# Optimization experiments

Measured on AMD Instinct MI355X. Metric: run time of the kernel, lower is better.

Reference implementation:

```python
import jax, jax.numpy as jnp
import numpy as np

OUT, IN, GS = 16384, 4096, 16
G = OUT * IN // GS  # 4194304 groups


def setup_inputs() -> dict:
    key = jax.random.key(0)
    k1, k2, k3, k4 = jax.random.split(key, 4)
    x = jax.random.normal(k1, (8, 32, IN), dtype=jnp.float32)
    weight_q2 = jax.random.randint(k2, (G, GS // 4), 0, 256, dtype=jnp.int32)
    weight_norm = jax.random.uniform(k3, (G, 1), dtype=jnp.float16)
    bias = jax.random.normal(k4, (OUT,), dtype=jnp.float32)
    return {"x": x, "weight_q2": weight_q2, "weight_norm": weight_norm, "bias": bias}


def _dequant_2bit(weight_q2, weight_norm):
    # torch: xq_out[:, i::4] = (xq >> 2i) & 3  =>  element index within group = i + 4*k
    # where k = packed column (slow, stride 4), i = shift index (fast).
    norm = weight_norm.astype(jnp.float32)                      # [G, 1]
    shifts = jnp.arange(4, dtype=jnp.int32) * 2                 # [4]
    vals = (weight_q2[:, :, None] >> shifts) & 3                # [G, 4(pack k), 4(shift i)]
    xq_out = vals.astype(jnp.float32).reshape(G, GS)            # [G, 16], layout k*4 + i
    w = (xq_out / 3.0) * (2.0 * norm) - norm                    # [G, 16]
    return w.reshape(OUT, IN)


def reference(x, weight_q2, weight_norm, bias):
    w = _dequant_2bit(weight_q2, weight_norm)                   # [OUT, IN] fp32
    return jnp.einsum('bsi,oi->bso', x, w) + bias
```

## Files before the change

kernel.cpp:

```cpp
#include <hip/hip_runtime.h>
#include <stdint.h>

#define M_DIM 256
#define N_DIM 16384
#define K_DIM 4096
#define BM 128
#define BN 64
#define BK 64

typedef __bf16 bf16x8 __attribute__((ext_vector_type(8)));
typedef float  f32x4  __attribute__((ext_vector_type(4)));

__device__ __forceinline__ uint32_t f2bf(float f) {
  uint32_t u = __float_as_uint(f);
  return (u + 0x7fffu + ((u >> 16) & 1u)) >> 16;
}

__global__ __launch_bounds__(256) void cvt_x_kernel(const float* __restrict__ x,
                                                    uint4* __restrict__ ws) {
  int T = blockIdx.x * 256 + threadIdx.x;
  int mb_glob = T >> 13;
  int r       = T & 8191;
  int kch     = r >> 6;
  int L       = r & 63;
  int row = mb_glob * 16 + (L & 15);
  int k   = kch * 32 + (L >> 4) * 8;
  const float* p = x + (size_t)row * K_DIM + k;
  float4 a = *(const float4*)p;
  float4 b = *(const float4*)(p + 4);
  uint4 o;
  o.x = f2bf(a.x) | (f2bf(a.y) << 16);
  o.y = f2bf(a.z) | (f2bf(a.w) << 16);
  o.z = f2bf(b.x) | (f2bf(b.y) << 16);
  o.w = f2bf(b.z) | (f2bf(b.w) << 16);
  ws[T] = o;
}

__global__ __launch_bounds__(256, 2) void gemm2bit_kernel(
    const uint4*    __restrict__ aws,
    const uint32_t* __restrict__ q2,
    const float*    __restrict__ nrm,
    const float*    __restrict__ bias,
    float*          __restrict__ out)
{
  __shared__ uint4 Ab[1024];
  __shared__ uint4 Bb[512];

  const int tid  = threadIdx.x;
  const int lane = tid & 63;
  const int w    = tid >> 6;
  const int wm   = w >> 1;
  const int wn   = w & 1;
  const int lo4  = lane & 15;
  const int qd   = lane >> 4;

  const int n0 = blockIdx.x * BN;
  const int m0 = blockIdx.y * BM;

  const int snb  = tid >> 6;
  const int sqd  = (tid >> 4) & 3;
  const int slo4 = tid & 15;
  const int grow = n0 + snb * 16 + slo4;

  f32x4 acc[4][2];
#pragma unroll
  for (int s = 0; s < 4; ++s)
#pragma unroll
    for (int u = 0; u < 2; ++u)
      acc[s][u] = (f32x4){0.f, 0.f, 0.f, 0.f};

  for (int kc = 0; kc < K_DIM; kc += BK) {
    __syncthreads();

#pragma unroll
    for (int j = 0; j < 4; ++j) {
      int s_lin = j * 256 + tid;
      int ca = s_lin >> 6;
      int L  = s_lin & 63;
      int ts = ca >> 3, mb = ca & 7;
      uint4 g = aws[((size_t)(blockIdx.y * 8 + mb) * 128 + (kc >> 5) + ts) * 64 + L];
      Ab[ca * 64 + L] = g;
    }

    {
      int gidx = grow * 256 + (kc >> 4) + sqd;
      uint4 q  = *(const uint4*)(q2 + (size_t)gidx * 4);
      float nv = nrm[gidx];
      float a  = nv * (2.0f / 3.0f);
      float b  = -nv;
      uint32_t res[8];
#pragma unroll
      for (int p = 0; p < 4; ++p) {
        uint32_t qq = (&q.x)[p];
        float f0 = fmaf((float)(qq & 3u), a, b);
        float f1 = fmaf((float)((qq >> 2) & 3u), a, b);
        float f2 = fmaf((float)((qq >> 4) & 3u), a, b);
        float f3 = fmaf((float)((qq >> 6) & 3u), a, b);
        res[p * 2]     = f2bf(f0) | (f2bf(f1) << 16);
        res[p * 2 + 1] = f2bf(f2) | (f2bf(f3) << 16);
      }
      int cb   = (sqd >> 1) * 4 + snb;
      int base = cb * 64 + (sqd & 1) * 32 + slo4;
      Bb[base]      = make_uint4(res[0], res[1], res[2], res[3]);
      Bb[base + 16] = make_uint4(res[4], res[5], res[6], res[7]);
    }

    __syncthreads();

#pragma unroll
    for (int ts = 0; ts < 2; ++ts) {
      bf16x8 af[4], bf[2];
#pragma unroll
      for (int s = 0; s < 4; ++s)
        af[s] = *(const bf16x8*)&Ab[(ts * 8 + wm * 4 + s) * 64 + lane];
#pragma unroll
      for (int u = 0; u < 2; ++u)
        bf[u] = *(const bf16x8*)&Bb[(ts * 4 + wn * 2 + u) * 64 + lane];
#pragma unroll
      for (int s = 0; s < 4; ++s)
#pragma unroll
        for (int u = 0; u < 2; ++u)
          acc[s][u] = __builtin_amdgcn_mfma_f32_16x16x32_bf16(
              af[s], bf[u], acc[s][u], 0, 0, 0);
    }
  }

  float bv[2];
#pragma unroll
  for (int u = 0; u < 2; ++u)
    bv[u] = bias[n0 + wn * 32 + u * 16 + lo4];

#pragma unroll
  for (int s = 0; s < 4; ++s) {
    int mrow = m0 + wm * 64 + s * 16 + qd * 4;
#pragma unroll
    for (int u = 0; u < 2; ++u) {
      int ncol = n0 + wn * 32 + u * 16 + lo4;
      float* p = out + (size_t)mrow * N_DIM + ncol;
#pragma unroll
      for (int r = 0; r < 4; ++r)
        p[(size_t)r * N_DIM] = acc[s][u][r] + bv[u];
    }
  }
}

extern "C" void kernel_launch(void* const* d_in, const int* in_sizes, int n_in,
                              void* d_out, int out_size, void* d_ws, size_t ws_size,
                              hipStream_t stream) {
  const float*    x    = (const float*)d_in[0];
  const uint32_t* q2   = (const uint32_t*)d_in[1];
  const float*    nm   = (const float*)d_in[2];
  const float*    bias = (const float*)d_in[3];
  float*          out  = (float*)d_out;
  uint4*          aws  = (uint4*)d_ws;

  cvt_x_kernel<<<512, 256, 0, stream>>>(x, aws);

  dim3 grid(N_DIM / BN, M_DIM / BM);
  gemm2bit_kernel<<<grid, 256, 0, stream>>>(aws, q2, nm, bias, out);
}
```

Measured before the change: 178.5 us.

## Double BK, register-prefetch next tile, and dequantize via byte-permute lookup

Doubles the K tile to 128 and prefetches the next iteration's activation and quantized weight loads into registers while the MFMAs run on the current tile, so global-load latency overlaps compute. The 2-bit dequantization changes from per-element int-to-float conversion, FMA and rounding to a precomputed bf16 lookup table of the four level values, indexed with v_perm byte selects. This adds register pressure from the prefetch buffers and doubles shared memory, which can lower occupancy. The lookup encodes the four levels as ±norm and ±norm/3 rounded to bf16 directly, which may differ slightly in rounding from the previous FMA path.

```diff
diff --git a/kernel.cpp b/kernel.cpp
--- a/kernel.cpp
+++ b/kernel.cpp
@@ -6,7 +6,8 @@
 #define K_DIM 4096
 #define BM 128
 #define BN 64
-#define BK 64
+#define BK 128
+#define NIT (K_DIM / BK)
 
 typedef __bf16 bf16x8 __attribute__((ext_vector_type(8)));
 typedef float  f32x4  __attribute__((ext_vector_type(4)));
@@ -43,24 +44,23 @@
     const float*    __restrict__ bias,
     float*          __restrict__ out)
 {
-  __shared__ uint4 Ab[1024];
-  __shared__ uint4 Bb[512];
+  __shared__ uint4 Ab[2048];
+  __shared__ uint4 Bb[1024];
 
   const int tid  = threadIdx.x;
-  const int lane = tid & 63;
+  const int l    = tid & 63;
   const int w    = tid >> 6;
   const int wm   = w >> 1;
   const int wn   = w & 1;
-  const int lo4  = lane & 15;
-  const int qd   = lane >> 4;
+  const int lo4  = l & 15;
+  const int qd   = l >> 4;
 
   const int n0 = blockIdx.x * BN;
   const int m0 = blockIdx.y * BM;
 
-  const int snb  = tid >> 6;
-  const int sqd  = (tid >> 4) & 3;
-  const int slo4 = tid & 15;
-  const int grow = n0 + snb * 16 + slo4;
+  const int srow = lo4 + w * 16;
+  const int sgk0 = qd;
+  const int grow = n0 + srow;
 
   f32x4 acc[4][2];
 #pragma unroll
@@ -69,53 +69,77 @@
     for (int u = 0; u < 2; ++u)
       acc[s][u] = (f32x4){0.f, 0.f, 0.f, 0.f};
 
-  for (int kc = 0; kc < K_DIM; kc += BK) {
-    __syncthreads();
+  uint4 pA[8];
+  uint4 pQ[2];
+  float pN[2];
 
+  const int mrow_base = blockIdx.y * 8;
+
+#define LOAD_A(IT)                                                          \
+  _Pragma("unroll") for (int j = 0; j < 8; ++j) {                           \
+    int s_lin = j * 256 + tid;                                              \
+    int c = s_lin >> 6, L = s_lin & 63;                                     \
+    pA[j] = aws[((size_t)(mrow_base + (c & 7)) * 128 + (IT)*4 + (c >> 3)) * 64 + L]; \
+  }
+#define LOAD_B(IT)                                                          \
+  _Pragma("unroll") for (int g = 0; g < 2; ++g) {                           \
+    int gidx = grow * 256 + (IT)*8 + sgk0 + 4 * g;                          \
+    pQ[g] = *(const uint4*)(q2 + (size_t)gidx * 4);                         \
+    pN[g] = nrm[gidx];                                                      \
+  }
+
+  LOAD_A(0)
+  LOAD_B(0)
+
+  for (int it = 0; it < NIT; ++it) {
+    uint32_t rw[16];
 #pragma unroll
-    for (int j = 0; j < 4; ++j) {
-      int s_lin = j * 256 + tid;
-      int ca = s_lin >> 6;
-      int L  = s_lin & 63;
-      int ts = ca >> 3, mb = ca & 7;
-      uint4 g = aws[((size_t)(blockIdx.y * 8 + mb) * 128 + (kc >> 5) + ts) * 64 + L];
-      Ab[ca * 64 + L] = g;
-    }
-
-    {
-      int gidx = grow * 256 + (kc >> 4) + sqd;
-      uint4 q  = *(const uint4*)(q2 + (size_t)gidx * 4);
-      float nv = nrm[gidx];
-      float a  = nv * (2.0f / 3.0f);
-      float b  = -nv;
-      uint32_t res[8];
+    for (int g = 0; g < 2; ++g) {
+      float nv = pN[g];
+      uint32_t u3 = f2bf(nv);
+      uint32_t u1 = f2bf(nv * 0.33333334f);
+      uint32_t T01 = (u3 | (u1 << 16)) ^ 0x80008000u;
+      uint32_t T23 = u1 | (u3 << 16);
 #pragma unroll
       for (int p = 0; p < 4; ++p) {
-        uint32_t qq = (&q.x)[p];
-        float f0 = fmaf((float)(qq & 3u), a, b);
-        float f1 = fmaf((float)((qq >> 2) & 3u), a, b);
-        float f2 = fmaf((float)((qq >> 4) & 3u), a, b);
-        float f3 = fmaf((float)((qq >> 6) & 3u), a, b);
-        res[p * 2]     = f2bf(f0) | (f2bf(f1) << 16);
-        res[p * 2 + 1] = f2bf(f2) | (f2bf(f3) << 16);
+        uint32_t qq = (&pQ[g].x)[p];
+        uint32_t v01 = (qq & 3u) | ((qq & 0x0Cu) << 14);
+        uint32_t v23 = ((qq >> 4) & 3u) | ((qq & 0xC0u) << 10);
+        rw[g * 8 + p * 2]     = __builtin_amdgcn_perm(T23, T01, v01 * 0x0202u + 0x01000100u);
+        rw[g * 8 + p * 2 + 1] = __builtin_amdgcn_perm(T23, T01, v23 * 0x0202u + 0x01000100u);
       }
-      int cb   = (sqd >> 1) * 4 + snb;
-      int base = cb * 64 + (sqd & 1) * 32 + slo4;
-      Bb[base]      = make_uint4(res[0], res[1], res[2], res[3]);
-      Bb[base + 16] = make_uint4(res[4], res[5], res[6], res[7]);
     }
 
     __syncthreads();
 
 #pragma unroll
-    for (int ts = 0; ts < 2; ++ts) {
+    for (int j = 0; j < 8; ++j)
+      Ab[j * 256 + tid] = pA[j];
+
+#pragma unroll
+    for (int g = 0; g < 2; ++g) {
+      int sgk  = sgk0 + 4 * g;
+      int base = ((sgk >> 1) * 4 + w) * 64 + (sgk & 1) * 32 + lo4;
+      Bb[base]      = make_uint4(rw[g * 8 + 0], rw[g * 8 + 1], rw[g * 8 + 2], rw[g * 8 + 3]);
+      Bb[base + 16] = make_uint4(rw[g * 8 + 4], rw[g * 8 + 5], rw[g * 8 + 6], rw[g * 8 + 7]);
+    }
+
+    __syncthreads();
+
+    if (it + 1 < NIT) {
+      LOAD_A(it + 1)
+      LOAD_B(it + 1)
+    }
+
+#pragma unroll
+    for (int ts = 0; ts < 4; ++ts) {
       bf16x8 af[4], bf[2];
 #pragma unroll
       for (int s = 0; s < 4; ++s)
-        af[s] = *(const bf16x8*)&Ab[(ts * 8 + wm * 4 + s) * 64 + lane];
+        af[s] = *(const bf16x8*)&Ab[(ts * 8 + wm * 4 + s) * 64 + l];
 #pragma unroll
       for (int u = 0; u < 2; ++u)
-        bf[u] = *(const bf16x8*)&Bb[(ts * 4 + wn * 2 + u) * 64 + lane];
+        bf[u] = *(const bf16x8*)&Bb[(ts * 4 + wn * 2 + u) * 64 + l];
 #pragma unroll
       for (int s = 0; s < 4; ++s)
 #pragma unroll
@@ -124,6 +148,8 @@
               af[s], bf[u], acc[s][u], 0, 0, 0);
     }
   }
+#undef LOAD_A
+#undef LOAD_B
 
   float bv[2];
 #pragma unroll
```

New measurement: 299.2 us. 1.68x slower.

## Prefetch next K-tile into registers and dequantize 2-bit weights via byte-permute lookup

Applied to the files above, without the earlier changes.

The loads for the next K tile of activations and packed weights are now issued into registers before the current tile's MFMA work, so global-memory latency overlaps with compute. The dequantization that did four FMAs plus bf16 rounding per weight is replaced by a table of four bf16 values (±norm, ±norm/3) built once per tile and selected with v_perm byte shuffles. This adds register pressure under launch bounds of 2 blocks per CU. The lookup's rounding of norm/3 may differ slightly from the original FMA path.

```diff
diff --git a/kernel.cpp b/kernel.cpp
--- a/kernel.cpp
+++ b/kernel.cpp
@@ -47,12 +47,12 @@
   __shared__ uint4 Bb[512];
 
   const int tid  = threadIdx.x;
-  const int lane = tid & 63;
+  const int l    = tid & 63;
   const int w    = tid >> 6;
   const int wm   = w >> 1;
   const int wn   = w & 1;
-  const int lo4  = lane & 15;
-  const int qd   = lane >> 4;
+  const int lo4  = l & 15;
+  const int qd   = l >> 4;
 
   const int n0 = blockIdx.x * BN;
   const int m0 = blockIdx.y * BM;
@@ -69,53 +69,72 @@
     for (int u = 0; u < 2; ++u)
       acc[s][u] = (f32x4){0.f, 0.f, 0.f, 0.f};
 
+  uint4 pA[4];
+  uint4 pQ;
+  float pN;
+
+#define LOAD_B(KC)                                              \
+  {                                                             \
+    int gidx = grow * 256 + ((KC) >> 4) + sqd;                  \
+    pQ = *(const uint4*)(q2 + (size_t)gidx * 4);                \
+    pN = nrm[gidx];                                             \
+  }
+#define LOAD_A(KC)                                                            \
+  _Pragma("unroll") for (int j = 0; j < 4; ++j) {                             \
+    int s_lin = j * 256 + tid;                                                \
+    int ca = s_lin >> 6, L = s_lin & 63;                                      \
+    pA[j] = aws[((size_t)(blockIdx.y * 8 + (ca & 7)) * 128 + ((KC) >> 5) +    \
+                 (ca >> 3)) * 64 + L];                                        \
+  }
+
+  LOAD_B(0)
+  LOAD_A(0)
+
   for (int kc = 0; kc < K_DIM; kc += BK) {
+    uint32_t rw[8];
+    {
+      uint32_t u3 = f2bf(pN);
+      uint32_t u1 = f2bf(pN * 0.33333334f);
+      uint32_t T01 = (u3 | (u1 << 16)) ^ 0x80008000u;
+      uint32_t T23 = u1 | (u3 << 16);
+#pragma unroll
+      for (int p = 0; p < 4; ++p) {
+        uint32_t qq = (&pQ.x)[p];
+        uint32_t v01 = (qq & 3u) | ((qq & 0x0Cu) << 14);
+        uint32_t v23 = ((qq >> 4) & 3u) | ((qq & 0xC0u) << 10);
+        rw[p * 2]     = __builtin_amdgcn_perm(T23, T01, v01 * 0x0202u + 0x01000100u);
+        rw[p * 2 + 1] = __builtin_amdgcn_perm(T23, T01, v23 * 0x0202u + 0x01000100u);
+      }
+    }
+
     __syncthreads();
 
 #pragma unroll
-    for (int j = 0; j < 4; ++j) {
-      int s_lin = j * 256 + tid;
-      int ca = s_lin >> 6;
-      int L  = s_lin & 63;
-      int ts = ca >> 3, mb = ca & 7;
-      uint4 g = aws[((size_t)(blockIdx.y * 8 + mb) * 128 + (kc >> 5) + ts) * 64 + L];
-      Ab[ca * 64 + L] = g;
-    }
+    for (int j = 0; j < 4; ++j)
+      Ab[j * 256 + tid] = pA[j];
 
     {
-      int gidx = grow * 256 + (kc >> 4) + sqd;
-      uint4 q  = *(const uint4*)(q2 + (size_t)gidx * 4);
-      float nv = nrm[gidx];
-      float a  = nv * (2.0f / 3.0f);
-      float b  = -nv;
-      uint32_t res[8];
-#pragma unroll
-      for (int p = 0; p < 4; ++p) {
-        uint32_t qq = (&q.x)[p];
-        float f0 = fmaf((float)(qq & 3u), a, b);
-        float f1 = fmaf((float)((qq >> 2) & 3u), a, b);
-        float f2 = fmaf((float)((qq >> 4) & 3u), a, b);
-        float f3 = fmaf((float)((qq >> 6) & 3u), a, b);
-        res[p * 2]     = f2bf(f0) | (f2bf(f1) << 16);
-        res[p * 2 + 1] = f2bf(f2) | (f2bf(f3) << 16);
-      }
-      int cb   = (sqd >> 1) * 4 + snb;
-      int base = cb * 64 + (sqd & 1) * 32 + slo4;
-      Bb[base]      = make_uint4(res[0], res[1], res[2], res[3]);
-      Bb[base + 16] = make_uint4(res[4], res[5], res[6], res[7]);
+      int base = ((sqd >> 1) * 4 + snb) * 64 + (sqd & 1) * 32 + slo4;
+      Bb[base]      = make_uint4(rw[0], rw[1], rw[2], rw[3]);
+      Bb[base + 16] = make_uint4(rw[4], rw[5], rw[6], rw[7]);
     }
 
     __syncthreads();
+
+    if (kc + BK < K_DIM) {
+      LOAD_B(kc + BK)
+      LOAD_A(kc + BK)
+    }
 
 #pragma unroll
     for (int ts = 0; ts < 2; ++ts) {
       bf16x8 af[4], bf[2];
 #pragma unroll
       for (int s = 0; s < 4; ++s)
-        af[s] = *(const bf16x8*)&Ab[(ts * 8 + wm * 4 + s) * 64 + lane];
+        af[s] = *(const bf16x8*)&Ab[(ts * 8 + wm * 4 + s) * 64 + l];
 #pragma unroll
       for (int u = 0; u < 2; ++u)
-        bf[u] = *(const bf16x8*)&Bb[(ts * 4 + wn * 2 + u) * 64 + lane];
+        bf[u] = *(const bf16x8*)&Bb[(ts * 4 + wn * 2 + u) * 64 + l];
 #pragma unroll
       for (int s = 0; s < 4; ++s)
 #pragma unroll
@@ -124,6 +143,8 @@
               af[s], bf[u], acc[s][u], 0, 0, 0);
     }
   }
+#undef LOAD_A
+#undef LOAD_B
 
   float bv[2];
 #pragma unroll
```

Measured after the change: 278.6 us. 56.1% more time.

## Split K across blocks with atomic accumulation and LUT-based 2-bit dequant

Applied to the files above, without the earlier changes.

Adds a split-K of 2 over a third grid dimension, so each block handles half the K range and accumulates into the zero-initialised output with float atomicAdd, with only the first slice adding bias. The fp32 FMA-plus-bf16-rounding dequant is replaced by a byte-permute lookup into a precomputed table of the four bf16 values (-n, -n/3, n/3, n). Launch bounds are raised to 4 blocks per SM. This aims to double block count and cut dequant ALU work, at the cost of a memset, atomic traffic, and a second read of A rows across slices.

```diff
diff --git a/kernel.cpp b/kernel.cpp
--- a/kernel.cpp
+++ b/kernel.cpp
@@ -7,6 +7,8 @@
 #define BM 128
 #define BN 64
 #define BK 64
+#define KSPLIT 2
+#define KSLICE (K_DIM / KSPLIT)
 
 typedef __bf16 bf16x8 __attribute__((ext_vector_type(8)));
 typedef float  f32x4  __attribute__((ext_vector_type(4)));
@@ -36,7 +38,7 @@
   ws[T] = o;
 }
 
-__global__ __launch_bounds__(256, 2) void gemm2bit_kernel(
+__global__ __launch_bounds__(256, 4) void gemm2bit_kernel(
     const uint4*    __restrict__ aws,
     const uint32_t* __restrict__ q2,
     const float*    __restrict__ nrm,
@@ -47,15 +49,16 @@
   __shared__ uint4 Bb[512];
 
   const int tid  = threadIdx.x;
-  const int lane = tid & 63;
+  const int l    = tid & 63;
   const int w    = tid >> 6;
   const int wm   = w >> 1;
   const int wn   = w & 1;
-  const int lo4  = lane & 15;
-  const int qd   = lane >> 4;
+  const int lo4  = l & 15;
+  const int qd   = l >> 4;
 
-  const int n0 = blockIdx.x * BN;
-  const int m0 = blockIdx.y * BM;
+  const int n0    = blockIdx.x * BN;
+  const int m0    = blockIdx.y * BM;
+  const int kbase = blockIdx.z * KSLICE;
 
   const int snb  = tid >> 6;
   const int sqd  = (tid >> 4) & 3;
@@ -69,7 +72,7 @@
     for (int u = 0; u < 2; ++u)
       acc[s][u] = (f32x4){0.f, 0.f, 0.f, 0.f};
 
-  for (int kc = 0; kc < K_DIM; kc += BK) {
+  for (int kc = kbase; kc < kbase + KSLICE; kc += BK) {
     __syncthreads();
 
 #pragma unroll
@@ -77,8 +80,8 @@
       int s_lin = j * 256 + tid;
       int ca = s_lin >> 6;
       int L  = s_lin & 63;
-      int ts = ca >> 3, mb = ca & 7;
-      uint4 g = aws[((size_t)(blockIdx.y * 8 + mb) * 128 + (kc >> 5) + ts) * 64 + L];
+      uint4 g = aws[((size_t)(blockIdx.y * 8 + (ca & 7)) * 128 + (kc >> 5) +
+                     (ca >> 3)) * 64 + L];
       Ab[ca * 64 + L] = g;
     }
 
@@ -86,23 +89,22 @@
       int gidx = grow * 256 + (kc >> 4) + sqd;
       uint4 q  = *(const uint4*)(q2 + (size_t)gidx * 4);
       float nv = nrm[gidx];
-      float a  = nv * (2.0f / 3.0f);
-      float b  = -nv;
-      uint32_t res[8];
+      uint32_t u3 = f2bf(nv);
+      uint32_t u1 = f2bf(nv * 0.33333334f);
+      uint32_t T01 = (u3 | (u1 << 16)) ^ 0x80008000u;
+      uint32_t T23 = u1 | (u3 << 16);
+      uint32_t rw[8];
 #pragma unroll
       for (int p = 0; p < 4; ++p) {
         uint32_t qq = (&q.x)[p];
-        float f0 = fmaf((float)(qq & 3u), a, b);
-        float f1 = fmaf((float)((qq >> 2) & 3u), a, b);
-        float f2 = fmaf((float)((qq >> 4) & 3u), a, b);
-        float f3 = fmaf((float)((qq >> 6) & 3u), a, b);
-        res[p * 2]     = f2bf(f0) | (f2bf(f1) << 16);
-        res[p * 2 + 1] = f2bf(f2) | (f2bf(f3) << 16);
+        uint32_t v01 = (qq & 3u) | ((qq & 0x0Cu) << 14);
+        uint32_t v23 = ((qq >> 4) & 3u) | ((qq & 0xC0u) << 10);
+        rw[p * 2]     = __builtin_amdgcn_perm(T23, T01, v01 * 0x0202u + 0x01000100u);
+        rw[p * 2 + 1] = __builtin_amdgcn_perm(T23, T01, v23 * 0x0202u + 0x01000100u);
       }
-      int cb   = (sqd >> 1) * 4 + snb;
-      int base = cb * 64 + (sqd & 1) * 32 + slo4;
-      Bb[base]      = make_uint4(res[0], res[1], res[2], res[3]);
-      Bb[base + 16] = make_uint4(res[4], res[5], res[6], res[7]);
+      int base = ((sqd >> 1) * 4 + snb) * 64 + (sqd & 1) * 32 + slo4;
+      Bb[base]      = make_uint4(rw[0], rw[1], rw[2], rw[3]);
+      Bb[base + 16] = make_uint4(rw[4], rw[5], rw[6], rw[7]);
     }
 
     __syncthreads();
@@ -112,10 +114,10 @@
       bf16x8 af[4], bf[2];
 #pragma unroll
       for (int s = 0; s < 4; ++s)
-        af[s] = *(const bf16x8*)&Ab[(ts * 8 + wm * 4 + s) * 64 + lane];
+        af[s] = *(const bf16x8*)&Ab[(ts * 8 + wm * 4 + s) * 64 + l];
 #pragma unroll
       for (int u = 0; u < 2; ++u)
-        bf[u] = *(const bf16x8*)&Bb[(ts * 4 + wn * 2 + u) * 64 + lane];
+        bf[u] = *(const bf16x8*)&Bb[(ts * 4 + wn * 2 + u) * 64 + l];
 #pragma unroll
       for (int s = 0; s < 4; ++s)
 #pragma unroll
@@ -128,7 +130,7 @@
   float bv[2];
 #pragma unroll
   for (int u = 0; u < 2; ++u)
-    bv[u] = bias[n0 + wn * 32 + u * 16 + lo4];
+    bv[u] = (blockIdx.z == 0) ? bias[n0 + wn * 32 + u * 16 + lo4] : 0.0f;
 
 #pragma unroll
   for (int s = 0; s < 4; ++s) {
@@ -139,7 +141,7 @@
       float* p = out + (size_t)mrow * N_DIM + ncol;
 #pragma unroll
       for (int r = 0; r < 4; ++r)
-        p[(size_t)r * N_DIM] = acc[s][u][r] + bv[u];
+        atomicAdd(p + (size_t)r * N_DIM, acc[s][u][r] + bv[u]);
     }
   }
 }
@@ -154,8 +156,10 @@
   float*          out  = (float*)d_out;
   uint4*          aws  = (uint4*)d_ws;
 
+  hipMemsetAsync(d_out, 0, (size_t)out_size * sizeof(float), stream);
+
   cvt_x_kernel<<<512, 256, 0, stream>>>(x, aws);
 
-  dim3 grid(N_DIM / BN, M_DIM / BM);
+  dim3 grid(N_DIM / BN, M_DIM / BM, KSPLIT);
   gemm2bit_kernel<<<grid, 256, 0, stream>>>(aws, q2, nm, bias, out);
 }
```

New measurement: 180.3 us. Within noise of the previous version (+1.0%).
